# Performance work log

Hardware: AMD Instinct MI355X
Metric: run time of the kernel (lower is better)

## Reference

```python
import jax, jax.numpy as jnp
import numpy as np

N_NODES = 50000
N_EDGES = 800000
F_IN = 64
HID = 64
N_CLASSES = 10
N_GRAPHS = 64


def setup_inputs() -> dict:
    key = jax.random.key(0)
    ks = jax.random.split(key, 16)
    x = jax.random.normal(ks[0], (N_NODES, F_IN), dtype=jnp.float32)
    edge_index = jax.random.randint(ks[1], (2, N_EDGES), 0, N_NODES, dtype=jnp.int32)
    supernode_mask = jax.random.bernoulli(ks[2], 0.1, (N_NODES,))
    edge_mask = jax.random.bernoulli(ks[3], 0.5, (N_EDGES,)).astype(jnp.float32)
    batch = jnp.sort(jax.random.randint(ks[4], (N_NODES,), 0, N_GRAPHS, dtype=jnp.int32))
    def glorot(k, fan_in, fan_out):
        s = jnp.sqrt(6.0 / (fan_in + fan_out))
        return jax.random.uniform(k, (fan_in, fan_out), jnp.float32, -s, s)
    W1 = glorot(ks[5], F_IN, HID); b1 = jnp.zeros((HID,), jnp.float32)
    W2 = glorot(ks[6], HID, HID); b2 = jnp.zeros((HID,), jnp.float32)
    W3 = glorot(ks[7], HID, HID); b3 = jnp.zeros((HID,), jnp.float32)
    Wl = glorot(ks[8], HID, N_CLASSES); bl = jnp.zeros((N_CLASSES,), jnp.float32)
    return {"x": x, "edge_index": edge_index, "supernode_mask": supernode_mask,
            "edge_mask": edge_mask, "batch": batch,
            "W1": W1, "b1": b1, "W2": W2, "b2": b2, "W3": W3, "b3": b3,
            "Wl": Wl, "bl": bl}


def reference(x, edge_index, supernode_mask, edge_mask, batch,
              W1, b1, W2, b2, W3, b3, Wl, bl):
    N = x.shape[0]
    src, dst = edge_index[0], edge_index[1]

    # SimpleConv('add'): weighted sum of source features into targets
    x2 = jax.ops.segment_sum(x[src] * edge_mask[:, None], dst, num_segments=N)
    x = jnp.where(supernode_mask[:, None], x2, x)

    # GCN normalization with self-loops: deg = 1 + in-degree, norm = d^-1/2[src]*d^-1/2[dst]
    deg = jax.ops.segment_sum(jnp.ones((src.shape[0],), x.dtype), dst, num_segments=N) + 1.0
    dinv = jax.lax.rsqrt(deg)
    coef = dinv[src] * dinv[dst]          # [E]
    self_coef = (dinv * dinv)[:, None]    # self-loop contribution [N,1]

    def gcn(h, W, b):
        h = h @ W  # small GEMM [N, HID]
        agg = jax.ops.segment_sum(h[src] * coef[:, None], dst, num_segments=N)
        return agg + h * self_coef + b

    h = jax.nn.relu(gcn(x, W1, b1))
    h = jax.nn.relu(gcn(h, W2, b2))
    h = gcn(h, W3, b3)

    # global_mean_pool over graphs
    sums = jax.ops.segment_sum(h, batch, num_segments=N_GRAPHS)
    cnt = jax.ops.segment_sum(jnp.ones((N,), h.dtype), batch, num_segments=N_GRAPHS)
    pooled = sums / jnp.maximum(cnt, 1.0)[:, None]

    # dropout is identity in eval mode
    return pooled @ Wl + bl
```

## Files before the change

kernel.cpp:

```cpp
#include <hip/hip_runtime.h>

#define FEAT 64
#define NGRAPH 64
#define POOL_CHUNKS 8
#define CAP 96
#define FILL_CHUNKS 128

typedef short bf16x8 __attribute__((ext_vector_type(8)));
typedef float f32x4 __attribute__((ext_vector_type(4)));
union FragU { uint4 u4; bf16x8 h; };


__device__ __forceinline__ unsigned int pack_bf16(float a, float b) {
    unsigned int ua = __float_as_uint(a), ub = __float_as_uint(b);
    ua = (ua + 0x7FFFu + ((ua >> 16) & 1u)) >> 16;
    ub = (ub + 0x7FFFu + ((ub >> 16) & 1u)) >> 16;
    return ua | (ub << 16);
}
__device__ __forceinline__ float bf_lo(unsigned int w) {
    return __uint_as_float(w << 16);
}
__device__ __forceinline__ float bf_hi(unsigned int w) {
    return __uint_as_float(w & 0xFFFF0000u);
}
__device__ __forceinline__ bool read_mask(const void* sm, int i, int fl) {
    if (fl & 2) return ((const float*)sm)[i] != 0.f;
    if (fl & 1) return ((const unsigned char*)sm)[i] != 0;
    return ((const int*)sm)[i] != 0;
}
__device__ __forceinline__ int lbound(const int* a, int n, int key) {
    int lo = 0, hi = n;
    while (lo < hi) {
        int mid = (lo + hi) >> 1;
        if (a[mid] < key) lo = mid + 1; else hi = mid;
    }
    return lo;
}

__global__ __launch_bounds__(256) void k_prep(const float* __restrict__ x,
                                              unsigned int* __restrict__ u, int n8,
                                              const float* __restrict__ W1,
                                              const float* __restrict__ W2,
                                              const float* __restrict__ W3,
                                              unsigned int* __restrict__ wt,
                                              const unsigned int* __restrict__ m,
                                              int nwords, int* __restrict__ flag) {
    int t = blockIdx.x * 256 + threadIdx.x;
    if (t < n8) {
        const float4 a = *(const float4*)(x + (size_t)t * 8);
        const float4 b = *(const float4*)(x + (size_t)t * 8 + 4);
        uint4 p;
        p.x = pack_bf16(a.x, a.y);
        p.y = pack_bf16(a.z, a.w);
        p.z = pack_bf16(b.x, b.y);
        p.w = pack_bf16(b.z, b.w);
        *(uint4*)(u + (size_t)t * 4) = p;
    }
    if (t < 3 * 2048) {
        int mm = t >> 11, w = t & 2047;
        int c = w >> 5, kw = w & 31;
        const float* W = (mm == 0) ? W1 : ((mm == 1) ? W2 : W3);
        wt[t] = pack_bf16(W[(2 * kw) * 64 + c], W[(2 * kw + 1) * 64 + c]);
    }
    if (t < nwords) {
        unsigned int w = m[t];
        if (w == 0x3F800000u) atomicOr(flag, 2);
        else if (w > 1u) atomicOr(flag, 1);
    }
}

__global__ __launch_bounds__(256) void k_fill(const int* __restrict__ ei,
                                              const float* __restrict__ emask,
                                              int* __restrict__ cnt,
                                              unsigned int* __restrict__ csr,
                                              int E, int ce) {
    int p = blockIdx.x & 7;
    int e0 = (blockIdx.x >> 3) * ce;
    int e1 = min(e0 + ce, E);
    for (int e = e0 + threadIdx.x; e < e1; e += 256) {
        int dst = ei[E + e];
        if ((dst >> 13) != p) continue;
        int pos = atomicAdd(&cnt[dst], 1);
        if (pos < CAP) {
            unsigned int word = (unsigned int)ei[e];
            if (emask[e] != 0.f) word |= 0x10000u;
            csr[(size_t)dst * CAP + pos] = word;
        }
    }
}

__global__ __launch_bounds__(256) void k_sup(const float* __restrict__ x,
                                             const int* __restrict__ cnt,
                                             const unsigned int* __restrict__ csr,
                                             const void* __restrict__ sm,
                                             const int* __restrict__ flag,
                                             unsigned int* __restrict__ u, int N) {
    int t = blockIdx.x * 256 + threadIdx.x;
    int i = t >> 6, lane = t & 63;
    if (i >= N) return;
    int fl = *flag;
    if (!read_mask(sm, i, fl)) return;
    int g = lane >> 4, q = lane & 15;
    int cn = min(cnt[i], CAP);
    const unsigned int* row = csr + (size_t)i * CAP;
    float4 acc = {0.f, 0.f, 0.f, 0.f};
    for (int j0 = 0; j0 < cn; j0 += 64) {
        int c = min(64, cn - j0);
        unsigned int w_l = (lane < c) ? row[j0 + lane] : 0u;
        int rounds4 = (c + 3) & ~3;
#pragma unroll 2
        for (int j = 0; j < rounds4; j += 4) {
            unsigned int wd = __shfl(w_l, j + g);
            if (wd & 0x10000u) {
                int s = (int)(wd & 0xFFFFu);
                const float4 v = *(const float4*)(x + (size_t)s * FEAT + q * 4);
                acc.x += v.x; acc.y += v.y; acc.z += v.z; acc.w += v.w;
            }
        }
    }
#pragma unroll
    for (int m = 16; m < 64; m <<= 1) {
        acc.x += __shfl_xor(acc.x, m);
        acc.y += __shfl_xor(acc.y, m);
        acc.z += __shfl_xor(acc.z, m);
        acc.w += __shfl_xor(acc.w, m);
    }
    if (g == 0) {
        uint2 p;
        p.x = pack_bf16(acc.x, acc.y);
        p.y = pack_bf16(acc.z, acc.w);
        *(uint2*)(u + (size_t)i * 32 + q * 2) = p;
    }
}

__global__ __launch_bounds__(256) void k_gemm_mfma(const unsigned int* __restrict__ u_in,
                                                   const unsigned int* __restrict__ wbfT,
                                                   const int* __restrict__ cnt,
                                                   unsigned int* __restrict__ hd, int N) {
    int wid = threadIdx.x >> 6, lane = threadIdx.x & 63;
    int row0 = (blockIdx.x * 4 + wid) * 16;
    if (row0 >= N) return;
    int r = lane & 15, half = lane >> 4;
    f32x4 acc0 = {0.f, 0.f, 0.f, 0.f}, acc1 = acc0, acc2 = acc0, acc3 = acc0;
#pragma unroll
    for (int ks = 0; ks < 2; ++ks) {
        FragU a;
        a.u4 = *(const uint4*)(u_in + (size_t)(row0 + r) * 32 + ks * 16 + half * 4);
        FragU b0, b1, b2, b3;
        b0.u4 = *(const uint4*)(wbfT + (0 * 16 + r) * 32 + ks * 16 + half * 4);
        b1.u4 = *(const uint4*)(wbfT + (1 * 16 + r) * 32 + ks * 16 + half * 4);
        b2.u4 = *(const uint4*)(wbfT + (2 * 16 + r) * 32 + ks * 16 + half * 4);
        b3.u4 = *(const uint4*)(wbfT + (3 * 16 + r) * 32 + ks * 16 + half * 4);
        acc0 = __builtin_amdgcn_mfma_f32_16x16x32_bf16(a.h, b0.h, acc0, 0, 0, 0);
        acc1 = __builtin_amdgcn_mfma_f32_16x16x32_bf16(a.h, b1.h, acc1, 0, 0, 0);
        acc2 = __builtin_amdgcn_mfma_f32_16x16x32_bf16(a.h, b2.h, acc2, 0, 0, 0);
        acc3 = __builtin_amdgcn_mfma_f32_16x16x32_bf16(a.h, b3.h, acc3, 0, 0, 0);
    }
    float dd0 = rsqrtf((float)cnt[row0 + half * 4 + 0] + 1.f);
    float dd1 = rsqrtf((float)cnt[row0 + half * 4 + 1] + 1.f);
    float dd2 = rsqrtf((float)cnt[row0 + half * 4 + 2] + 1.f);
    float dd3 = rsqrtf((float)cnt[row0 + half * 4 + 3] + 1.f);
#pragma unroll
    for (int t = 0; t < 4; ++t) {
        const f32x4 acc = (t == 0) ? acc0 : (t == 1) ? acc1 : (t == 2) ? acc2 : acc3;
        float v0 = acc[0] * dd0, v1 = acc[1] * dd1, v2 = acc[2] * dd2, v3 = acc[3] * dd3;
        float o0 = __shfl_xor(v0, 1), o1 = __shfl_xor(v1, 1),
              o2 = __shfl_xor(v2, 1), o3 = __shfl_xor(v3, 1);
        if ((r & 1) == 0) {
            size_t base = (size_t)(row0 + half * 4) * 32 + t * 8 + (r >> 1);
            hd[base + 0 * 32] = pack_bf16(v0, o0);
            hd[base + 1 * 32] = pack_bf16(v1, o1);
            hd[base + 2 * 32] = pack_bf16(v2, o2);
            hd[base + 3 * 32] = pack_bf16(v3, o3);
        }
    }
}

__global__ __launch_bounds__(256) void k_gather(const unsigned int* __restrict__ hd,
                                                const float* __restrict__ b,
                                                const int* __restrict__ cnt,
                                                const unsigned int* __restrict__ csr,
                                                unsigned int* __restrict__ u_out,
                                                int N, int do_relu) {
    int t = blockIdx.x * 256 + threadIdx.x;
    int i = t >> 6, lane = t & 63;
    if (i >= N) return;
    int g = lane >> 3, q = lane & 7;
    int cn = cnt[i];
    int r1 = min(cn, CAP);
    const unsigned int* row = csr + (size_t)i * CAP;
    float acc[8] = {0.f, 0.f, 0.f, 0.f, 0.f, 0.f, 0.f, 0.f};
    for (int j0 = 0; j0 < r1; j0 += 64) {
        int c = min(64, r1 - j0);
        int s_l = (lane < c) ? (int)(row[j0 + lane] & 0xFFFFu) : 0;
        int rounds8 = (c + 7) & ~7;
#pragma unroll 2
        for (int j = 0; j < rounds8; j += 8) {
            int jj = j + g;
            int s = __shfl(s_l, jj);
            if (jj < c) {
                const uint4 v = *(const uint4*)(hd + (size_t)s * 32 + q * 4);
                acc[0] += bf_lo(v.x); acc[1] += bf_hi(v.x);
                acc[2] += bf_lo(v.y); acc[3] += bf_hi(v.y);
                acc[4] += bf_lo(v.z); acc[5] += bf_hi(v.z);
                acc[6] += bf_lo(v.w); acc[7] += bf_hi(v.w);
            }
        }
    }
#pragma unroll
    for (int m = 8; m < 64; m <<= 1) {
#pragma unroll
        for (int k = 0; k < 8; ++k) acc[k] += __shfl_xor(acc[k], m);
    }
    if (g == 0) {
        float dd = rsqrtf((float)cn + 1.f);
        const uint4 hv = *(const uint4*)(hd + (size_t)i * 32 + q * 4);
        const float4 b0 = *(const float4*)(b + q * 8);
        const float4 b1 = *(const float4*)(b + q * 8 + 4);
        float r[8];
        r[0] = (acc[0] + bf_lo(hv.x)) * dd + b0.x;
        r[1] = (acc[1] + bf_hi(hv.x)) * dd + b0.y;
        r[2] = (acc[2] + bf_lo(hv.y)) * dd + b0.z;
        r[3] = (acc[3] + bf_hi(hv.y)) * dd + b0.w;
        r[4] = (acc[4] + bf_lo(hv.z)) * dd + b1.x;
        r[5] = (acc[5] + bf_hi(hv.z)) * dd + b1.y;
        r[6] = (acc[6] + bf_lo(hv.w)) * dd + b1.z;
        r[7] = (acc[7] + bf_hi(hv.w)) * dd + b1.w;
        if (do_relu) {
#pragma unroll
            for (int k = 0; k < 8; ++k) r[k] = fmaxf(r[k], 0.f);
        }
        uint4 p;
        p.x = pack_bf16(r[0], r[1]);
        p.y = pack_bf16(r[2], r[3]);
        p.z = pack_bf16(r[4], r[5]);
        p.w = pack_bf16(r[6], r[7]);
        *(uint4*)(u_out + (size_t)i * 32 + q * 4) = p;
    }
}

__global__ __launch_bounds__(256) void k_pool(const unsigned int* __restrict__ xb,
                                              const int* __restrict__ batch,
                                              float* __restrict__ pooled, int N) {
    int g = blockIdx.x >> 3, c = blockIdx.x & (POOL_CHUNKS - 1);
    int lo = lbound(batch, N, g);
    int hi = lbound(batch, N, g + 1);
    int len = hi - lo;
    int t = threadIdx.x, lane = t & 63, sub = t >> 6;
    int a = lo + (int)(((long long)len * c) / POOL_CHUNKS);
    int bnd = lo + (int)(((long long)len * (c + 1)) / POOL_CHUNKS);
    float s = 0.f;
    int w = lane >> 1;
    bool hi_half = lane & 1;
    for (int i = a + sub; i < bnd; i += 4) {
        unsigned int word = xb[(size_t)i * 32 + w];
        s += hi_half ? bf_hi(word) : bf_lo(word);
    }
    __shared__ float red[4][64];
    red[sub][lane] = s;
    __syncthreads();
    if (sub == 0) {
        float tot = red[0][lane] + red[1][lane] + red[2][lane] + red[3][lane];
        unsafeAtomicAdd(&pooled[g * FEAT + lane], tot);
    }
}

__global__ __launch_bounds__(640) void k_logits(const float* __restrict__ pooled,
                                                const int* __restrict__ batch, int N,
                                                const float* __restrict__ Wl,
                                                const float* __restrict__ bl,
                                                float* __restrict__ out) {
    __shared__ float inv[NGRAPH];
    int t = threadIdx.x;
    if (t < NGRAPH) {
        int lo = lbound(batch, N, t);
        int hi = lbound(batch, N, t + 1);
        inv[t] = 1.f / fmaxf((float)(hi - lo), 1.f);
    }
    __syncthreads();
    if (t >= NGRAPH * 10) return;
    int g = t / 10, cls = t % 10;
    float s = 0.f;
#pragma unroll
    for (int f = 0; f < 64; ++f) s += pooled[g * 64 + f] * Wl[f * 10 + cls];
    out[t] = s * inv[g] + bl[cls];
}

extern "C" void kernel_launch(void* const* d_in, const int* in_sizes, int n_in,
                              void* d_out, int out_size, void* d_ws, size_t ws_size,
                              hipStream_t stream) {
    const float* x = (const float*)d_in[0];
    const int* ei = (const int*)d_in[1];
    const void* sm = d_in[2];
    const float* emask = (const float*)d_in[3];
    const int* batch = (const int*)d_in[4];
    const float* W1 = (const float*)d_in[5];
    const float* b1 = (const float*)d_in[6];
    const float* W2 = (const float*)d_in[7];
    const float* b2 = (const float*)d_in[8];
    const float* W3 = (const float*)d_in[9];
    const float* b3 = (const float*)d_in[10];
    const float* Wl = (const float*)d_in[11];
    const float* bl = (const float*)d_in[12];

    const int N = in_sizes[0] / FEAT;
    const int E = in_sizes[1] / 2;

    float* wsf = (float*)d_ws;
    size_t off = 0;
    unsigned int* ua = (unsigned int*)(wsf + off); off += (size_t)N * 32;
    unsigned int* ub = (unsigned int*)(wsf + off); off += (size_t)N * 32;
    unsigned int* hd = (unsigned int*)(wsf + off); off += (size_t)N * 32;
    unsigned int* wbf = (unsigned int*)(wsf + off); off += 3 * 2048;
    unsigned int* csr = (unsigned int*)(wsf + off); off += (size_t)N * CAP;
    int* cnt_int = (int*)(wsf + off);  off += N;
    float* pooled = wsf + off;         off += NGRAPH * FEAT;
    int* flag = (int*)(wsf + off);     off += 1;

    const int wblocks = (N * 64 + 255) / 256;
    const int gemm_blocks = (N / 16 + 3) / 4;
    const int prep_blocks = (N * 8 + 255) / 256;
    const int ce = (E + FILL_CHUNKS - 1) / FILL_CHUNKS;

    hipMemsetAsync(cnt_int, 0, (size_t)(N + NGRAPH * FEAT + 1) * 4, stream);
    k_prep<<<prep_blocks, 256, 0, stream>>>(x, ua, N * 8, W1, W2, W3, wbf,
                                            (const unsigned int*)sm, N / 4, flag);
    k_fill<<<FILL_CHUNKS * 8, 256, 0, stream>>>(ei, emask, cnt_int, csr, E, ce);
    k_sup<<<wblocks, 256, 0, stream>>>(x, cnt_int, csr, sm, flag, ua, N);

    k_gemm_mfma<<<gemm_blocks, 256, 0, stream>>>(ua, wbf + 0 * 2048, cnt_int, hd, N);
    k_gather<<<wblocks, 256, 0, stream>>>(hd, b1, cnt_int, csr, ub, N, 1);
    k_gemm_mfma<<<gemm_blocks, 256, 0, stream>>>(ub, wbf + 1 * 2048, cnt_int, hd, N);
    k_gather<<<wblocks, 256, 0, stream>>>(hd, b2, cnt_int, csr, ua, N, 1);
    k_gemm_mfma<<<gemm_blocks, 256, 0, stream>>>(ua, wbf + 2 * 2048, cnt_int, hd, N);
    k_gather<<<wblocks, 256, 0, stream>>>(hd, b3, cnt_int, csr, ub, N, 0);

    k_pool<<<NGRAPH * POOL_CHUNKS, 256, 0, stream>>>(ub, batch, pooled, N);
    k_logits<<<1, 640, 0, stream>>>(pooled, batch, N, Wl, bl, (float*)d_out);
}
```

Measured before the change: 200.5 us.

## Partition CSR rows by edge mask and shrink indices to 16 bits

The fill kernel now packs the masked and unmasked in-degree counts into one 32-bit counter. Masked-in edges go at the front of each CSR row and masked-out edges at the back, and source indices are stored as 16-bit values. The supernode kernel then walks only the front segment instead of testing a flag per entry, and the gather kernels read two contiguous segments with half the index bytes. Fill chunk count is also doubled. Truncating indices to 16 bits relies on node ids below 65536 (N is 50000), and the packed counts assume per-node degrees fit in 16 bits.

```diff
diff --git a/kernel.cpp b/kernel.cpp
--- a/kernel.cpp
+++ b/kernel.cpp
@@ -4,7 +4,7 @@
 #define NGRAPH 64
 #define POOL_CHUNKS 8
 #define CAP 96
-#define FILL_CHUNKS 128
+#define FILL_CHUNKS 256
 
 typedef short bf16x8 __attribute__((ext_vector_type(8)));
 typedef float f32x4 __attribute__((ext_vector_type(4)));
@@ -71,8 +71,8 @@
 
 __global__ __launch_bounds__(256) void k_fill(const int* __restrict__ ei,
                                               const float* __restrict__ emask,
-                                              int* __restrict__ cnt,
-                                              unsigned int* __restrict__ csr,
+                                              unsigned int* __restrict__ cnt,
+                                              unsigned short* __restrict__ csr,
                                               int E, int ce) {
     int p = blockIdx.x & 7;
     int e0 = (blockIdx.x >> 3) * ce;
@@ -80,18 +80,22 @@
     for (int e = e0 + threadIdx.x; e < e1; e += 256) {
         int dst = ei[E + e];
         if ((dst >> 13) != p) continue;
-        int pos = atomicAdd(&cnt[dst], 1);
-        if (pos < CAP) {
-            unsigned int word = (unsigned int)ei[e];
-            if (emask[e] != 0.f) word |= 0x10000u;
-            csr[(size_t)dst * CAP + pos] = word;
+        bool w = emask[e] != 0.f;
+        unsigned int old = atomicAdd(&cnt[dst], w ? 1u : 0x10000u);
+        unsigned short s = (unsigned short)ei[e];
+        if (w) {
+            unsigned int f = old & 0xFFFFu;
+            if (f < CAP) csr[(size_t)dst * CAP + f] = s;
+        } else {
+            unsigned int b = old >> 16;
+            if (b < CAP) csr[(size_t)dst * CAP + (CAP - 1 - b)] = s;
         }
     }
 }
 
 __global__ __launch_bounds__(256) void k_sup(const float* __restrict__ x,
-                                             const int* __restrict__ cnt,
-                                             const unsigned int* __restrict__ csr,
+                                             const unsigned int* __restrict__ cnt,
+                                             const unsigned short* __restrict__ csr,
                                              const void* __restrict__ sm,
                                              const int* __restrict__ flag,
                                              unsigned int* __restrict__ u, int N) {
@@ -101,18 +105,19 @@
     int fl = *flag;
     if (!read_mask(sm, i, fl)) return;
     int g = lane >> 4, q = lane & 15;
-    int cn = min(cnt[i], CAP);
-    const unsigned int* row = csr + (size_t)i * CAP;
+    int f = (int)(cnt[i] & 0xFFFFu);
+    f = min(f, CAP);
+    const unsigned short* row = csr + (size_t)i * CAP;
     float4 acc = {0.f, 0.f, 0.f, 0.f};
-    for (int j0 = 0; j0 < cn; j0 += 64) {
-        int c = min(64, cn - j0);
-        unsigned int w_l = (lane < c) ? row[j0 + lane] : 0u;
+    for (int j0 = 0; j0 < f; j0 += 64) {
+        int c = min(64, f - j0);
+        int s_l = (lane < c) ? (int)row[j0 + lane] : 0;
         int rounds4 = (c + 3) & ~3;
 #pragma unroll 2
         for (int j = 0; j < rounds4; j += 4) {
-            unsigned int wd = __shfl(w_l, j + g);
-            if (wd & 0x10000u) {
-                int s = (int)(wd & 0xFFFFu);
+            int jj = j + g;
+            int s = __shfl(s_l, jj);
+            if (jj < c) {
                 const float4 v = *(const float4*)(x + (size_t)s * FEAT + q * 4);
                 acc.x += v.x; acc.y += v.y; acc.z += v.z; acc.w += v.w;
             }
@@ -135,7 +140,7 @@
 
 __global__ __launch_bounds__(256) void k_gemm_mfma(const unsigned int* __restrict__ u_in,
                                                    const unsigned int* __restrict__ wbfT,
-                                                   const int* __restrict__ cnt,
+                                                   const unsigned int* __restrict__ cnt,
                                                    unsigned int* __restrict__ hd, int N) {
     int wid = threadIdx.x >> 6, lane = threadIdx.x & 63;
     int row0 = (blockIdx.x * 4 + wid) * 16;
@@ -156,10 +161,12 @@
         acc2 = __builtin_amdgcn_mfma_f32_16x16x32_bf16(a.h, b2.h, acc2, 0, 0, 0);
         acc3 = __builtin_amdgcn_mfma_f32_16x16x32_bf16(a.h, b3.h, acc3, 0, 0, 0);
     }
-    float dd0 = rsqrtf((float)cnt[row0 + half * 4 + 0] + 1.f);
-    float dd1 = rsqrtf((float)cnt[row0 + half * 4 + 1] + 1.f);
-    float dd2 = rsqrtf((float)cnt[row0 + half * 4 + 2] + 1.f);
-    float dd3 = rsqrtf((float)cnt[row0 + half * 4 + 3] + 1.f);
+    unsigned int c0 = cnt[row0 + half * 4 + 0], c1 = cnt[row0 + half * 4 + 1];
+    unsigned int c2 = cnt[row0 + half * 4 + 2], c3 = cnt[row0 + half * 4 + 3];
+    float dd0 = rsqrtf((float)((c0 & 0xFFFFu) + (c0 >> 16)) + 1.f);
+    float dd1 = rsqrtf((float)((c1 & 0xFFFFu) + (c1 >> 16)) + 1.f);
+    float dd2 = rsqrtf((float)((c2 & 0xFFFFu) + (c2 >> 16)) + 1.f);
+    float dd3 = rsqrtf((float)((c3 & 0xFFFFu) + (c3 >> 16)) + 1.f);
 #pragma unroll
     for (int t = 0; t < 4; ++t) {
         const f32x4 acc = (t == 0) ? acc0 : (t == 1) ? acc1 : (t == 2) ? acc2 : acc3;
@@ -176,23 +183,14 @@
     }
 }
 
-__global__ __launch_bounds__(256) void k_gather(const unsigned int* __restrict__ hd,
-                                                const float* __restrict__ b,
-                                                const int* __restrict__ cnt,
-                                                const unsigned int* __restrict__ csr,
-                                                unsigned int* __restrict__ u_out,
-                                                int N, int do_relu) {
-    int t = blockIdx.x * 256 + threadIdx.x;
-    int i = t >> 6, lane = t & 63;
-    if (i >= N) return;
-    int g = lane >> 3, q = lane & 7;
-    int cn = cnt[i];
-    int r1 = min(cn, CAP);
-    const unsigned int* row = csr + (size_t)i * CAP;
-    float acc[8] = {0.f, 0.f, 0.f, 0.f, 0.f, 0.f, 0.f, 0.f};
-    for (int j0 = 0; j0 < r1; j0 += 64) {
-        int c = min(64, r1 - j0);
-        int s_l = (lane < c) ? (int)(row[j0 + lane] & 0xFFFFu) : 0;
+__device__ __forceinline__ void gather_seg(const unsigned short* __restrict__ row,
+                                           int base, int cnt_seg,
+                                           const unsigned int* __restrict__ hd,
+                                           int lane, int g, int q,
+                                           float* __restrict__ acc) {
+    for (int j0 = 0; j0 < cnt_seg; j0 += 64) {
+        int c = min(64, cnt_seg - j0);
+        int s_l = (lane < c) ? (int)row[base + j0 + lane] : 0;
         int rounds8 = (c + 7) & ~7;
 #pragma unroll 2
         for (int j = 0; j < rounds8; j += 8) {
@@ -207,13 +205,35 @@
             }
         }
     }
+}
+
+__global__ __launch_bounds__(256) void k_gather(const unsigned int* __restrict__ hd,
+                                                const float* __restrict__ b,
+                                                const unsigned int* __restrict__ cnt,
+                                                const unsigned short* __restrict__ csr,
+                                                unsigned int* __restrict__ u_out,
+                                                int N, int do_relu) {
+    int t = blockIdx.x * 256 + threadIdx.x;
+    int i = t >> 6, lane = t & 63;
+    if (i >= N) return;
+    int g = lane >> 3, q = lane & 7;
+    unsigned int cw = cnt[i];
+    int f = (int)(cw & 0xFFFFu);
+    int bk = (int)(cw >> 16);
+    int deg = f + bk;
+    f = min(f, CAP);
+    bk = min(bk, CAP - f);
+    const unsigned short* row = csr + (size_t)i * CAP;
+    float acc[8] = {0.f, 0.f, 0.f, 0.f, 0.f, 0.f, 0.f, 0.f};
+    gather_seg(row, 0, f, hd, lane, g, q, acc);
+    gather_seg(row, CAP - bk, bk, hd, lane, g, q, acc);
 #pragma unroll
     for (int m = 8; m < 64; m <<= 1) {
 #pragma unroll
         for (int k = 0; k < 8; ++k) acc[k] += __shfl_xor(acc[k], m);
     }
     if (g == 0) {
-        float dd = rsqrtf((float)cn + 1.f);
+        float dd = rsqrtf((float)deg + 1.f);
         const uint4 hv = *(const uint4*)(hd + (size_t)i * 32 + q * 4);
         const float4 b0 = *(const float4*)(b + q * 8);
         const float4 b1 = *(const float4*)(b + q * 8 + 4);
@@ -312,8 +332,8 @@
     unsigned int* ub = (unsigned int*)(wsf + off); off += (size_t)N * 32;
     unsigned int* hd = (unsigned int*)(wsf + off); off += (size_t)N * 32;
     unsigned int* wbf = (unsigned int*)(wsf + off); off += 3 * 2048;
-    unsigned int* csr = (unsigned int*)(wsf + off); off += (size_t)N * CAP;
-    int* cnt_int = (int*)(wsf + off);  off += N;
+    unsigned short* csr = (unsigned short*)(wsf + off); off += (size_t)N * CAP / 2;
+    unsigned int* cnt_u = (unsigned int*)(wsf + off); off += N;
     float* pooled = wsf + off;         off += NGRAPH * FEAT;
     int* flag = (int*)(wsf + off);     off += 1;
 
@@ -322,18 +342,18 @@
     const int prep_blocks = (N * 8 + 255) / 256;
     const int ce = (E + FILL_CHUNKS - 1) / FILL_CHUNKS;
 
-    hipMemsetAsync(cnt_int, 0, (size_t)(N + NGRAPH * FEAT + 1) * 4, stream);
+    hipMemsetAsync(cnt_u, 0, (size_t)(N + NGRAPH * FEAT + 1) * 4, stream);
     k_prep<<<prep_blocks, 256, 0, stream>>>(x, ua, N * 8, W1, W2, W3, wbf,
                                             (const unsigned int*)sm, N / 4, flag);
-    k_fill<<<FILL_CHUNKS * 8, 256, 0, stream>>>(ei, emask, cnt_int, csr, E, ce);
-    k_sup<<<wblocks, 256, 0, stream>>>(x, cnt_int, csr, sm, flag, ua, N);
-
-    k_gemm_mfma<<<gemm_blocks, 256, 0, stream>>>(ua, wbf + 0 * 2048, cnt_int, hd, N);
-    k_gather<<<wblocks, 256, 0, stream>>>(hd, b1, cnt_int, csr, ub, N, 1);
-    k_gemm_mfma<<<gemm_blocks, 256, 0, stream>>>(ub, wbf + 1 * 2048, cnt_int, hd, N);
-    k_gather<<<wblocks, 256, 0, stream>>>(hd, b2, cnt_int, csr, ua, N, 1);
-    k_gemm_mfma<<<gemm_blocks, 256, 0, stream>>>(ua, wbf + 2 * 2048, cnt_int, hd, N);
-    k_gather<<<wblocks, 256, 0, stream>>>(hd, b3, cnt_int, csr, ub, N, 0);
+    k_fill<<<FILL_CHUNKS * 8, 256, 0, stream>>>(ei, emask, cnt_u, csr, E, ce);
+    k_sup<<<wblocks, 256, 0, stream>>>(x, cnt_u, csr, sm, flag, ua, N);
+
+    k_gemm_mfma<<<gemm_blocks, 256, 0, stream>>>(ua, wbf + 0 * 2048, cnt_u, hd, N);
+    k_gather<<<wblocks, 256, 0, stream>>>(hd, b1, cnt_u, csr, ub, N, 1);
+    k_gemm_mfma<<<gemm_blocks, 256, 0, stream>>>(ub, wbf + 1 * 2048, cnt_u, hd, N);
+    k_gather<<<wblocks, 256, 0, stream>>>(hd, b2, cnt_u, csr, ua, N, 1);
+    k_gemm_mfma<<<gemm_blocks, 256, 0, stream>>>(ua, wbf + 2 * 2048, cnt_u, hd, N);
+    k_gather<<<wblocks, 256, 0, stream>>>(hd, b3, cnt_u, csr, ub, N, 0);
 
     k_pool<<<NGRAPH * POOL_CHUNKS, 256, 0, stream>>>(ub, batch, pooled, N);
     k_logits<<<1, 640, 0, stream>>>(pooled, batch, N, Wl, bl, (float*)d_out);
```

Measured after the change: 209.6 us. +4.5%, slower.

## Split per-node edge counters into four sub-buckets and fuse fill with prep

Applied to the files above, without the earlier changes.

Each destination now has four atomic counters chosen by edge index mod 4, each owning a 24-slot sub-bucket of the CSR row. The aim is to spread atomic contention on high-degree nodes, and consumers remap a compact index across the sub-buckets. The fill and prep kernels are merged into one launch, and the fill grid is doubled. The cost is more counter memory, uint4 count loads, and index remapping in the gather kernels. Per-bucket overflow can also drop edges earlier than the old global cap of 96 did.

```diff
diff --git a/kernel.cpp b/kernel.cpp
--- a/kernel.cpp
+++ b/kernel.cpp
@@ -4,7 +4,9 @@
 #define NGRAPH 64
 #define POOL_CHUNKS 8
 #define CAP 96
-#define FILL_CHUNKS 128
+#define SUB 24
+#define FILL_CHUNKS 256
+#define FILLB (FILL_CHUNKS * 8)
 
 typedef short bf16x8 __attribute__((ext_vector_type(8)));
 typedef float f32x4 __attribute__((ext_vector_type(4)));
@@ -37,15 +39,38 @@
     return lo;
 }
 
-__global__ __launch_bounds__(256) void k_prep(const float* __restrict__ x,
-                                              unsigned int* __restrict__ u, int n8,
-                                              const float* __restrict__ W1,
-                                              const float* __restrict__ W2,
-                                              const float* __restrict__ W3,
-                                              unsigned int* __restrict__ wt,
-                                              const unsigned int* __restrict__ m,
-                                              int nwords, int* __restrict__ flag) {
-    int t = blockIdx.x * 256 + threadIdx.x;
+__global__ __launch_bounds__(256) void k_fillprep(const int* __restrict__ ei,
+                                                  const float* __restrict__ emask,
+                                                  unsigned int* __restrict__ cnt,
+                                                  unsigned int* __restrict__ csr,
+                                                  int E, int ce,
+                                                  const float* __restrict__ x,
+                                                  unsigned int* __restrict__ u, int n8,
+                                                  const float* __restrict__ W1,
+                                                  const float* __restrict__ W2,
+                                                  const float* __restrict__ W3,
+                                                  unsigned int* __restrict__ wt,
+                                                  const unsigned int* __restrict__ m,
+                                                  int nwords, int* __restrict__ flag) {
+    int bid = blockIdx.x;
+    if (bid < FILLB) {
+        int p = bid & 7;
+        int e0 = (bid >> 3) * ce;
+        int e1 = min(e0 + ce, E);
+        for (int e = e0 + (int)threadIdx.x; e < e1; e += 256) {
+            int dst = ei[E + e];
+            if ((dst >> 13) != p) continue;
+            int ph = e & 3;
+            unsigned int slot = atomicAdd(&cnt[dst * 4 + ph], 1u);
+            if (slot < SUB) {
+                unsigned int word = (unsigned int)ei[e];
+                if (emask[e] != 0.f) word |= 0x10000u;
+                csr[(size_t)dst * CAP + ph * SUB + slot] = word;
+            }
+        }
+        return;
+    }
+    int t = (bid - FILLB) * 256 + threadIdx.x;
     if (t < n8) {
         const float4 a = *(const float4*)(x + (size_t)t * 8);
         const float4 b = *(const float4*)(x + (size_t)t * 8 + 4);
@@ -69,28 +94,15 @@
     }
 }
 
-__global__ __launch_bounds__(256) void k_fill(const int* __restrict__ ei,
-                                              const float* __restrict__ emask,
-                                              int* __restrict__ cnt,
-                                              unsigned int* __restrict__ csr,
-                                              int E, int ce) {
-    int p = blockIdx.x & 7;
-    int e0 = (blockIdx.x >> 3) * ce;
-    int e1 = min(e0 + ce, E);
-    for (int e = e0 + threadIdx.x; e < e1; e += 256) {
-        int dst = ei[E + e];
-        if ((dst >> 13) != p) continue;
-        int pos = atomicAdd(&cnt[dst], 1);
-        if (pos < CAP) {
-            unsigned int word = (unsigned int)ei[e];
-            if (emask[e] != 0.f) word |= 0x10000u;
-            csr[(size_t)dst * CAP + pos] = word;
-        }
-    }
+__device__ __forceinline__ int vmap(int vj, int p1, int p2, int p3) {
+    return (vj < p1) ? vj
+         : (vj < p2) ? SUB + (vj - p1)
+         : (vj < p3) ? 2 * SUB + (vj - p2)
+         : 3 * SUB + (vj - p3);
 }
 
 __global__ __launch_bounds__(256) void k_sup(const float* __restrict__ x,
-                                             const int* __restrict__ cnt,
+                                             const uint4* __restrict__ cnt4,
                                              const unsigned int* __restrict__ csr,
                                              const void* __restrict__ sm,
                                              const int* __restrict__ flag,
@@ -101,12 +113,16 @@
     int fl = *flag;
     if (!read_mask(sm, i, fl)) return;
     int g = lane >> 4, q = lane & 15;
-    int cn = min(cnt[i], CAP);
+    uint4 c4 = cnt4[i];
+    int l0 = min((int)c4.x, SUB), l1 = min((int)c4.y, SUB);
+    int l2 = min((int)c4.z, SUB), l3 = min((int)c4.w, SUB);
+    int p1 = l0, p2 = l0 + l1, p3 = p2 + l2;
+    int tot = p3 + l3;
     const unsigned int* row = csr + (size_t)i * CAP;
     float4 acc = {0.f, 0.f, 0.f, 0.f};
-    for (int j0 = 0; j0 < cn; j0 += 64) {
-        int c = min(64, cn - j0);
-        unsigned int w_l = (lane < c) ? row[j0 + lane] : 0u;
+    for (int j0 = 0; j0 < tot; j0 += 64) {
+        int c = min(64, tot - j0);
+        unsigned int w_l = (lane < c) ? row[vmap(j0 + lane, p1, p2, p3)] : 0u;
         int rounds4 = (c + 3) & ~3;
 #pragma unroll 2
         for (int j = 0; j < rounds4; j += 4) {
@@ -135,7 +151,7 @@
 
 __global__ __launch_bounds__(256) void k_gemm_mfma(const unsigned int* __restrict__ u_in,
                                                    const unsigned int* __restrict__ wbfT,
-                                                   const int* __restrict__ cnt,
+                                                   const uint4* __restrict__ cnt4,
                                                    unsigned int* __restrict__ hd, int N) {
     int wid = threadIdx.x >> 6, lane = threadIdx.x & 63;
     int row0 = (blockIdx.x * 4 + wid) * 16;
@@ -156,10 +172,12 @@
         acc2 = __builtin_amdgcn_mfma_f32_16x16x32_bf16(a.h, b2.h, acc2, 0, 0, 0);
         acc3 = __builtin_amdgcn_mfma_f32_16x16x32_bf16(a.h, b3.h, acc3, 0, 0, 0);
     }
-    float dd0 = rsqrtf((float)cnt[row0 + half * 4 + 0] + 1.f);
-    float dd1 = rsqrtf((float)cnt[row0 + half * 4 + 1] + 1.f);
-    float dd2 = rsqrtf((float)cnt[row0 + half * 4 + 2] + 1.f);
-    float dd3 = rsqrtf((float)cnt[row0 + half * 4 + 3] + 1.f);
+    uint4 c0 = cnt4[row0 + half * 4 + 0], c1 = cnt4[row0 + half * 4 + 1];
+    uint4 c2 = cnt4[row0 + half * 4 + 2], c3 = cnt4[row0 + half * 4 + 3];
+    float dd0 = rsqrtf((float)(c0.x + c0.y + c0.z + c0.w) + 1.f);
+    float dd1 = rsqrtf((float)(c1.x + c1.y + c1.z + c1.w) + 1.f);
+    float dd2 = rsqrtf((float)(c2.x + c2.y + c2.z + c2.w) + 1.f);
+    float dd3 = rsqrtf((float)(c3.x + c3.y + c3.z + c3.w) + 1.f);
 #pragma unroll
     for (int t = 0; t < 4; ++t) {
         const f32x4 acc = (t == 0) ? acc0 : (t == 1) ? acc1 : (t == 2) ? acc2 : acc3;
@@ -178,7 +196,7 @@
 
 __global__ __launch_bounds__(256) void k_gather(const unsigned int* __restrict__ hd,
                                                 const float* __restrict__ b,
-                                                const int* __restrict__ cnt,
+                                                const uint4* __restrict__ cnt4,
                                                 const unsigned int* __restrict__ csr,
                                                 unsigned int* __restrict__ u_out,
                                                 int N, int do_relu) {
@@ -186,13 +204,17 @@
     int i = t >> 6, lane = t & 63;
     if (i >= N) return;
     int g = lane >> 3, q = lane & 7;
-    int cn = cnt[i];
-    int r1 = min(cn, CAP);
+    uint4 c4 = cnt4[i];
+    int deg = (int)(c4.x + c4.y + c4.z + c4.w);
+    int l0 = min((int)c4.x, SUB), l1 = min((int)c4.y, SUB);
+    int l2 = min((int)c4.z, SUB), l3 = min((int)c4.w, SUB);
+    int p1 = l0, p2 = l0 + l1, p3 = p2 + l2;
+    int tot = p3 + l3;
     const unsigned int* row = csr + (size_t)i * CAP;
     float acc[8] = {0.f, 0.f, 0.f, 0.f, 0.f, 0.f, 0.f, 0.f};
-    for (int j0 = 0; j0 < r1; j0 += 64) {
-        int c = min(64, r1 - j0);
-        int s_l = (lane < c) ? (int)(row[j0 + lane] & 0xFFFFu) : 0;
+    for (int j0 = 0; j0 < tot; j0 += 64) {
+        int c = min(64, tot - j0);
+        int s_l = (lane < c) ? (int)(row[vmap(j0 + lane, p1, p2, p3)] & 0xFFFFu) : 0;
         int rounds8 = (c + 7) & ~7;
 #pragma unroll 2
         for (int j = 0; j < rounds8; j += 8) {
@@ -213,7 +235,7 @@
         for (int k = 0; k < 8; ++k) acc[k] += __shfl_xor(acc[k], m);
     }
     if (g == 0) {
-        float dd = rsqrtf((float)cn + 1.f);
+        float dd = rsqrtf((float)deg + 1.f);
         const uint4 hv = *(const uint4*)(hd + (size_t)i * 32 + q * 4);
         const float4 b0 = *(const float4*)(b + q * 8);
         const float4 b1 = *(const float4*)(b + q * 8 + 4);
@@ -313,7 +335,7 @@
     unsigned int* hd = (unsigned int*)(wsf + off); off += (size_t)N * 32;
     unsigned int* wbf = (unsigned int*)(wsf + off); off += 3 * 2048;
     unsigned int* csr = (unsigned int*)(wsf + off); off += (size_t)N * CAP;
-    int* cnt_int = (int*)(wsf + off);  off += N;
+    unsigned int* cnt = (unsigned int*)(wsf + off); off += (size_t)N * 4;
     float* pooled = wsf + off;         off += NGRAPH * FEAT;
     int* flag = (int*)(wsf + off);     off += 1;
 
@@ -322,18 +344,18 @@
     const int prep_blocks = (N * 8 + 255) / 256;
     const int ce = (E + FILL_CHUNKS - 1) / FILL_CHUNKS;
 
-    hipMemsetAsync(cnt_int, 0, (size_t)(N + NGRAPH * FEAT + 1) * 4, stream);
-    k_prep<<<prep_blocks, 256, 0, stream>>>(x, ua, N * 8, W1, W2, W3, wbf,
-                                            (const unsigned int*)sm, N / 4, flag);
-    k_fill<<<FILL_CHUNKS * 8, 256, 0, stream>>>(ei, emask, cnt_int, csr, E, ce);
-    k_sup<<<wblocks, 256, 0, stream>>>(x, cnt_int, csr, sm, flag, ua, N);
-
-    k_gemm_mfma<<<gemm_blocks, 256, 0, stream>>>(ua, wbf + 0 * 2048, cnt_int, hd, N);
-    k_gather<<<wblocks, 256, 0, stream>>>(hd, b1, cnt_int, csr, ub, N, 1);
-    k_gemm_mfma<<<gemm_blocks, 256, 0, stream>>>(ub, wbf + 1 * 2048, cnt_int, hd, N);
-    k_gather<<<wblocks, 256, 0, stream>>>(hd, b2, cnt_int, csr, ua, N, 1);
-    k_gemm_mfma<<<gemm_blocks, 256, 0, stream>>>(ua, wbf + 2 * 2048, cnt_int, hd, N);
-    k_gather<<<wblocks, 256, 0, stream>>>(hd, b3, cnt_int, csr, ub, N, 0);
+    hipMemsetAsync(cnt, 0, (size_t)(N * 4 + NGRAPH * FEAT + 1) * 4, stream);
+    k_fillprep<<<FILLB + prep_blocks, 256, 0, stream>>>(
+        ei, emask, cnt, csr, E, ce,
+        x, ua, N * 8, W1, W2, W3, wbf, (const unsigned int*)sm, N / 4, flag);
+    k_sup<<<wblocks, 256, 0, stream>>>(x, (const uint4*)cnt, csr, sm, flag, ua, N);
+
+    k_gemm_mfma<<<gemm_blocks, 256, 0, stream>>>(ua, wbf + 0 * 2048, (const uint4*)cnt, hd, N);
+    k_gather<<<wblocks, 256, 0, stream>>>(hd, b1, (const uint4*)cnt, csr, ub, N, 1);
+    k_gemm_mfma<<<gemm_blocks, 256, 0, stream>>>(ub, wbf + 1 * 2048, (const uint4*)cnt, hd, N);
+    k_gather<<<wblocks, 256, 0, stream>>>(hd, b2, (const uint4*)cnt, csr, ua, N, 1);
+    k_gemm_mfma<<<gemm_blocks, 256, 0, stream>>>(ua, wbf + 2 * 2048, (const uint4*)cnt, hd, N);
+    k_gather<<<wblocks, 256, 0, stream>>>(hd, b3, (const uint4*)cnt, csr, ub, N, 0);
 
     k_pool<<<NGRAPH * POOL_CHUNKS, 256, 0, stream>>>(ub, batch, pooled, N);
     k_logits<<<1, 640, 0, stream>>>(pooled, batch, N, Wl, bl, (float*)d_out);
```

Result: no change. 198.8 us (-0.8%).
